# Kernel optimization log

Measured on AMD Instinct MI355X. Metric: run time of the kernel, lower is better.

## Reference

```python
import jax, jax.numpy as jnp
import numpy as np

FACTOR = 1.0   # module's self.factor
EPS = 1e-6     # rmsnorm eps


def setup_inputs() -> dict:
    key = jax.random.key(0)
    k0, k1, k2, k3 = jax.random.split(key, 4)
    B, S = 4, 2048
    D_IN = D_STATE = D_OUT = 2048
    N_HEADS = 32
    HD = D_STATE // N_HEADS  # 64
    x = jax.random.normal(k0, (B, S, D_IN), jnp.float32)
    w_in = jax.random.normal(k1, (D_STATE, D_IN), jnp.float32) * 0.02
    b_in = jnp.zeros((D_STATE,), jnp.float32)
    state_weight = jax.random.normal(k2, (N_HEADS, HD, HD), jnp.float32) * 0.02
    norm_weight = jnp.ones((D_STATE,), jnp.float32)
    w_out = jax.random.normal(k3, (D_OUT, D_STATE), jnp.float32) * (0.02 / np.sqrt(2 * 24))
    return dict(x=x, w_in=w_in, b_in=b_in, state_weight=state_weight,
                norm_weight=norm_weight, w_out=w_out)


def _rnn_scan(xt, W):
    # xt: (B, S, N, H); W: (N, H, H)
    B, S, N, H = xt.shape

    def step(s, x_t):
        # s: (B, N, H) ; per-head linear recurrence with tanh nonlinearity
        s = jnp.tanh(jnp.einsum('bnh,nhk->bnk', s, W) + x_t)
        return s, s

    s0 = jnp.zeros((B, N, H), xt.dtype)
    _, states = jax.lax.scan(step, s0, jnp.swapaxes(xt, 0, 1))  # (S, B, N, H)
    return jnp.swapaxes(states, 0, 1)  # (B, S, N, H)


def reference(x, w_in, b_in, state_weight, norm_weight, w_out):
    B, S, _ = x.shape
    N, H, _ = state_weight.shape
    h = x @ w_in.T + b_in                      # input_projection: (B,S,state)
    h = h.reshape(B, S, N, H) * FACTOR
    W = state_weight * FACTOR
    states = _rnn_scan(h, W)                   # (B,S,N,H)
    y = states.reshape(B, S, N * H)
    # rmsnorm
    y = y * jax.lax.rsqrt(jnp.mean(y * y, axis=-1, keepdims=True) + EPS) * norm_weight
    return y @ w_out.T                         # output_projection (no bias)
```

## Files before the change

kernel.cpp:

```cpp
#include <hip/hip_runtime.h>
#include <hip/hip_bf16.h>
#include <cstdint>


typedef short bf16x8 __attribute__((ext_vector_type(8)));
typedef float f32x4 __attribute__((ext_vector_type(4)));
typedef _Float16 f16x2 __attribute__((ext_vector_type(2)));

#define GLD16(gp, lp)                                                          \
  __builtin_amdgcn_global_load_lds(                                            \
      (const __attribute__((address_space(1))) void*)(gp),                     \
      (__attribute__((address_space(3))) void*)(lp), 16, 0, 0)

__global__ __launch_bounds__(256) void cvt_f32_bf16(
    const float* __restrict__ in, __hip_bfloat16* __restrict__ out, int n4) {
  int i = blockIdx.x * 256 + threadIdx.x;
  if (i >= n4) return;
  float4 v = ((const float4*)in)[i];
  __hip_bfloat16 a = __float2bfloat16(v.x);
  __hip_bfloat16 b = __float2bfloat16(v.y);
  __hip_bfloat16 c = __float2bfloat16(v.z);
  __hip_bfloat16 d = __float2bfloat16(v.w);
  ushort4 p;
  p.x = *(unsigned short*)&a; p.y = *(unsigned short*)&b;
  p.z = *(unsigned short*)&c; p.w = *(unsigned short*)&d;
  ((ushort4*)out)[i] = p;
}

__global__ __launch_bounds__(256) void gemm_nt(
    const __hip_bfloat16* __restrict__ A, const __hip_bfloat16* __restrict__ B,
    const float* __restrict__ bias, float* __restrict__ C,
    int M, int N, int K) {
  __shared__ __hip_bfloat16 As[128 * 32];
  __shared__ __hip_bfloat16 Bs[128 * 32];
  const int tid  = threadIdx.x;
  const int lane = tid & 63;
  const int wave = tid >> 6;
  const int wm = wave >> 1, wn = wave & 1;
  const long bm = (long)blockIdx.y * 128;
  const long bn = (long)blockIdx.x * 128;

  const int c0 = tid, c1 = tid + 256;
  const int r0 = c0 >> 2, k0 = (c0 & 3) * 8;
  const int r1 = c1 >> 2, k1 = (c1 & 3) * 8;
  __hip_bfloat16* lA0 = &As[(wave * 64) * 8];
  __hip_bfloat16* lA1 = &As[(256 + wave * 64) * 8];
  __hip_bfloat16* lB0 = &Bs[(wave * 64) * 8];
  __hip_bfloat16* lB1 = &Bs[(256 + wave * 64) * 8];
  const __hip_bfloat16* gA0 = A + (bm + r0) * (long)K + k0;
  const __hip_bfloat16* gA1 = A + (bm + r1) * (long)K + k1;
  const __hip_bfloat16* gB0 = B + (bn + r0) * (long)K + k0;
  const __hip_bfloat16* gB1 = B + (bn + r1) * (long)K + k1;

  const int fr = lane & 15;
  const int fk = (lane >> 4) * 8;

  f32x4 acc[4][4];
#pragma unroll
  for (int i = 0; i < 4; i++)
#pragma unroll
    for (int j = 0; j < 4; j++) acc[i][j] = {0.f, 0.f, 0.f, 0.f};

  for (int kt = 0; kt < K; kt += 32) {
    __syncthreads();
    GLD16(gA0 + kt, lA0);
    GLD16(gA1 + kt, lA1);
    GLD16(gB0 + kt, lB0);
    GLD16(gB1 + kt, lB1);
    __syncthreads();
    bf16x8 af[4], bfr[4];
#pragma unroll
    for (int t = 0; t < 4; t++)
      af[t] = *(const bf16x8*)&As[(wm * 64 + t * 16 + fr) * 32 + fk];
#pragma unroll
    for (int t = 0; t < 4; t++)
      bfr[t] = *(const bf16x8*)&Bs[(wn * 64 + t * 16 + fr) * 32 + fk];
#pragma unroll
    for (int i = 0; i < 4; i++)
#pragma unroll
      for (int j = 0; j < 4; j++)
        acc[i][j] = __builtin_amdgcn_mfma_f32_16x16x32_bf16(
            af[i], bfr[j], acc[i][j], 0, 0, 0);
  }

  const int cr = (lane >> 4) * 4;
  const int cc = lane & 15;
#pragma unroll
  for (int j = 0; j < 4; j++) {
    const long n = bn + wn * 64 + j * 16 + cc;
    const float bv = bias ? bias[n] : 0.0f;
#pragma unroll
    for (int i = 0; i < 4; i++) {
      const long m = bm + wm * 64 + i * 16 + cr;
#pragma unroll
      for (int r = 0; r < 4; r++)
        C[(m + r) * (long)N + n] = acc[i][j][r] + bv;
    }
  }
}

__device__ __forceinline__ float tanh_fast(float z) {
  float e = __builtin_amdgcn_exp2f(z * 2.8853900817779268f);
  return 1.0f - 2.0f * __builtin_amdgcn_rcpf(e + 1.0f);
}

__global__ __launch_bounds__(64) void scan_kernel(
    const float* __restrict__ Wst, float* __restrict__ h) {
  const int b = blockIdx.x >> 5;
  const int n = blockIdx.x & 31;
  const int lane = threadIdx.x;
  const float* Wn = Wst + n * 4096;

  f16x2 w2[32];
#pragma unroll
  for (int j = 0; j < 32; j++) {
    f16x2 t;
    t.x = (_Float16)Wn[(2 * j) * 64 + lane];
    t.y = (_Float16)Wn[(2 * j + 1) * 64 + lane];
    w2[j] = t;
  }

  __shared__ alignas(16) unsigned short s_h[64];

  int4 sv[8];
#pragma unroll
  for (int q = 0; q < 8; q++) sv[q] = make_int4(0, 0, 0, 0);

  float* hp = h + ((size_t)b * 2048) * 2048 + n * 64 + lane;
  float xcur[8], xnxt[8];
#pragma unroll
  for (int i = 0; i < 8; i++) xcur[i] = hp[(size_t)i * 2048];

  for (int t0 = 0; t0 < 2048; t0 += 8) {
    if (t0 + 8 < 2048) {
#pragma unroll
      for (int i = 0; i < 8; i++)
        xnxt[i] = hp[(size_t)(t0 + 8 + i) * 2048];
    }
#pragma unroll
    for (int i = 0; i < 8; i++) {
      float a0 = xcur[i], a1 = 0.f, a2 = 0.f, a3 = 0.f;
#pragma unroll
      for (int q = 0; q < 8; q++) {
        a0 = __builtin_amdgcn_fdot2(__builtin_bit_cast(f16x2, sv[q].x),
                                    w2[4 * q + 0], a0, false);
        a1 = __builtin_amdgcn_fdot2(__builtin_bit_cast(f16x2, sv[q].y),
                                    w2[4 * q + 1], a1, false);
        a2 = __builtin_amdgcn_fdot2(__builtin_bit_cast(f16x2, sv[q].z),
                                    w2[4 * q + 2], a2, false);
        a3 = __builtin_amdgcn_fdot2(__builtin_bit_cast(f16x2, sv[q].w),
                                    w2[4 * q + 3], a3, false);
      }
      float z = (a0 + a1) + (a2 + a3);
      float sn = tanh_fast(z);
      _Float16 sh = (_Float16)sn;
      s_h[lane] = __builtin_bit_cast(unsigned short, sh);
#pragma unroll
      for (int q = 0; q < 8; q++) sv[q] = ((const int4*)s_h)[q];
      hp[(size_t)(t0 + i) * 2048] = sn;
    }
#pragma unroll
    for (int i = 0; i < 8; i++) xcur[i] = xnxt[i];
  }
}

__global__ __launch_bounds__(256) void rmsnorm_to_bf16(
    const float* __restrict__ Y, const float* __restrict__ g,
    __hip_bfloat16* __restrict__ O) {
  const long row = blockIdx.x;
  const float* yr = Y + row * 2048;
  const int tid = threadIdx.x;
  float4 v0 = ((const float4*)yr)[tid * 2];
  float4 v1 = ((const float4*)yr)[tid * 2 + 1];
  float ss = v0.x * v0.x + v0.y * v0.y + v0.z * v0.z + v0.w * v0.w +
             v1.x * v1.x + v1.y * v1.y + v1.z * v1.z + v1.w * v1.w;
#pragma unroll
  for (int off = 32; off > 0; off >>= 1) ss += __shfl_down(ss, off);
  __shared__ float red[4];
  if ((tid & 63) == 0) red[tid >> 6] = ss;
  __syncthreads();
  float inv = rsqrtf((red[0] + red[1] + red[2] + red[3]) * (1.0f / 2048.0f)
                     + 1e-6f);
  float4 g0 = ((const float4*)(g + tid * 8))[0];
  float4 g1 = ((const float4*)(g + tid * 8))[1];
  float ov[8] = {v0.x * inv * g0.x, v0.y * inv * g0.y,
                 v0.z * inv * g0.z, v0.w * inv * g0.w,
                 v1.x * inv * g1.x, v1.y * inv * g1.y,
                 v1.z * inv * g1.z, v1.w * inv * g1.w};
  ushort4 p0, p1;
  __hip_bfloat16 t;
  t = __float2bfloat16(ov[0]); p0.x = *(unsigned short*)&t;
  t = __float2bfloat16(ov[1]); p0.y = *(unsigned short*)&t;
  t = __float2bfloat16(ov[2]); p0.z = *(unsigned short*)&t;
  t = __float2bfloat16(ov[3]); p0.w = *(unsigned short*)&t;
  t = __float2bfloat16(ov[4]); p1.x = *(unsigned short*)&t;
  t = __float2bfloat16(ov[5]); p1.y = *(unsigned short*)&t;
  t = __float2bfloat16(ov[6]); p1.z = *(unsigned short*)&t;
  t = __float2bfloat16(ov[7]); p1.w = *(unsigned short*)&t;
  ushort4* op = (ushort4*)(O + row * 2048 + tid * 8);
  op[0] = p0;
  op[1] = p1;
}

extern "C" void kernel_launch(void* const* d_in, const int* in_sizes, int n_in,
                              void* d_out, int out_size, void* d_ws,
                              size_t ws_size, hipStream_t stream) {
  const float* x     = (const float*)d_in[0];
  const float* w_in  = (const float*)d_in[1];
  const float* b_in  = (const float*)d_in[2];
  const float* w_st  = (const float*)d_in[3];
  const float* nw    = (const float*)d_in[4];
  const float* w_out = (const float*)d_in[5];
  float* out = (float*)d_out;

  char* ws = (char*)d_ws;
  __hip_bfloat16* x_bf  = (__hip_bfloat16*)(ws);
  __hip_bfloat16* wi_bf = (__hip_bfloat16*)(ws + 33554432);
  __hip_bfloat16* wo_bf = (__hip_bfloat16*)(ws + 41943040);
  float* h              = (float*)(ws + 50331648);

  cvt_f32_bf16<<<16384, 256, 0, stream>>>(x, x_bf, 4194304);
  cvt_f32_bf16<<<4096, 256, 0, stream>>>(w_in, wi_bf, 1048576);
  cvt_f32_bf16<<<4096, 256, 0, stream>>>(w_out, wo_bf, 1048576);

  gemm_nt<<<dim3(16, 64), 256, 0, stream>>>(x_bf, wi_bf, b_in, h,
                                            8192, 2048, 2048);
  scan_kernel<<<128, 64, 0, stream>>>(w_st, h);
  rmsnorm_to_bf16<<<8192, 256, 0, stream>>>(h, nw, x_bf);
  gemm_nt<<<dim3(16, 64), 256, 0, stream>>>(x_bf, wo_bf, nullptr, out,
                                            8192, 2048, 2048);
}
```

Measured before the change: 760.8 us.

## Use packed fp16 FMA accumulation in scan and remap GEMM block order

The scan's inner dot products now accumulate in packed fp16 using elementwise FMA instead of fdot2 with fp32 accumulators. The partial sums are combined in fp16 and the input is added in fp32 only at the end. Separately, the GEMM remaps block IDs into strided chunks (column-major tile order) to change L2 locality and workgroup distribution. The fp16 accumulation cuts per-step latency on the serial recurrence but loses accuracy over 64-term sums, which may compound across the 2048-step scan.

Result: no change. 759.9 us (-0.1%).

```diff
diff --git a/kernel.cpp b/kernel.cpp
--- a/kernel.cpp
+++ b/kernel.cpp
@@ -37,8 +37,14 @@
   const int lane = tid & 63;
   const int wave = tid >> 6;
   const int wm = wave >> 1, wn = wave & 1;
-  const long bm = (long)blockIdx.y * 128;
-  const long bn = (long)blockIdx.x * 128;
+
+  const int id = blockIdx.y * gridDim.x + blockIdx.x;
+  const int chunk = (gridDim.x * gridDim.y) >> 3;
+  const int v = (id & 7) * chunk + (id >> 3);
+  const int vbn = v / gridDim.y;
+  const int vbm = v - vbn * gridDim.y;
+  const long bm = (long)vbm * 128;
+  const long bn = (long)vbn * 128;
 
   const int c0 = tid, c1 = tid + 256;
   const int r0 = c0 >> 2, k0 = (c0 & 3) * 8;
@@ -113,11 +119,11 @@
 
   f16x2 w2[32];
 #pragma unroll
-  for (int j = 0; j < 32; j++) {
+  for (int p = 0; p < 32; p++) {
     f16x2 t;
-    t.x = (_Float16)Wn[(2 * j) * 64 + lane];
-    t.y = (_Float16)Wn[(2 * j + 1) * 64 + lane];
-    w2[j] = t;
+    t.x = (_Float16)Wn[(2 * p) * 64 + lane];
+    t.y = (_Float16)Wn[(2 * p + 1) * 64 + lane];
+    w2[p] = t;
   }
 
   __shared__ alignas(16) unsigned short s_h[64];
@@ -130,6 +136,8 @@
   float xcur[8], xnxt[8];
 #pragma unroll
   for (int i = 0; i < 8; i++) xcur[i] = hp[(size_t)i * 2048];
+
+  const f16x2 z2 = {(_Float16)0.f, (_Float16)0.f};
 
   for (int t0 = 0; t0 < 2048; t0 += 8) {
     if (t0 + 8 < 2048) {
@@ -139,19 +147,22 @@
     }
 #pragma unroll
     for (int i = 0; i < 8; i++) {
-      float a0 = xcur[i], a1 = 0.f, a2 = 0.f, a3 = 0.f;
+      f16x2 ac0 = z2, ac1 = z2, ac2 = z2, ac3 = z2;
 #pragma unroll
       for (int q = 0; q < 8; q++) {
-        a0 = __builtin_amdgcn_fdot2(__builtin_bit_cast(f16x2, sv[q].x),
-                                    w2[4 * q + 0], a0, false);
-        a1 = __builtin_amdgcn_fdot2(__builtin_bit_cast(f16x2, sv[q].y),
-                                    w2[4 * q + 1], a1, false);
-        a2 = __builtin_amdgcn_fdot2(__builtin_bit_cast(f16x2, sv[q].z),
-                                    w2[4 * q + 2], a2, false);
-        a3 = __builtin_amdgcn_fdot2(__builtin_bit_cast(f16x2, sv[q].w),
-                                    w2[4 * q + 3], a3, false);
+        ac0 = __builtin_elementwise_fma(__builtin_bit_cast(f16x2, sv[q].x),
+                                        w2[4 * q + 0], ac0);
+        ac1 = __builtin_elementwise_fma(__builtin_bit_cast(f16x2, sv[q].y),
+                                        w2[4 * q + 1], ac1);
+        ac2 = __builtin_elementwise_fma(__builtin_bit_cast(f16x2, sv[q].z),
+                                        w2[4 * q + 2], ac2);
+        ac3 = __builtin_elementwise_fma(__builtin_bit_cast(f16x2, sv[q].w),
+                                        w2[4 * q + 3], ac3);
       }
-      float z = (a0 + a1) + (a2 + a3);
+      f16x2 p01 = ac0 + ac1;
+      f16x2 p23 = ac2 + ac3;
+      f16x2 pt = p01 + p23;
+      float z = (float)pt.x + (float)pt.y + xcur[i];
       float sn = tanh_fast(z);
       _Float16 sh = (_Float16)sn;
       s_h[lane] = __builtin_bit_cast(unsigned short, sh);
```
